# Kernel optimization log

Measured on AMD Instinct MI355X. Metric: run time of the kernel, lower is better.

The kernel has to match this reference:

```python
import jax, jax.numpy as jnp
import numpy as np

N = 50000
E = 1600000
F_IN = 4
F_OUT = 32
PERIODS = 12


def setup_inputs() -> dict:
    key = jax.random.key(0)
    ks = jax.random.split(key, 18)
    s_in = 1.0 / np.sqrt(F_IN)
    s_cat = 1.0 / np.sqrt(2 * F_OUT)
    s_out = 1.0 / np.sqrt(F_OUT)
    inp = {
        'x': jax.random.normal(ks[0], (N, F_IN, PERIODS), dtype=jnp.float32),
        'edge_index': jax.random.randint(ks[1], (2, E), 0, N, dtype=jnp.int32),
        'attention': jax.random.uniform(ks[2], (PERIODS,), dtype=jnp.float32),
        # GRU update gate z: GCNConv weight/bias + Linear(2*F_OUT -> F_OUT)
        'Wz': jax.random.normal(ks[3], (F_IN, F_OUT), jnp.float32) * s_in,
        'bz': jnp.zeros((F_OUT,), jnp.float32),
        'Lz': jax.random.normal(ks[4], (2 * F_OUT, F_OUT), jnp.float32) * s_cat,
        'lz': jnp.zeros((F_OUT,), jnp.float32),
        # reset gate r
        'Wr': jax.random.normal(ks[5], (F_IN, F_OUT), jnp.float32) * s_in,
        'br': jnp.zeros((F_OUT,), jnp.float32),
        'Lr': jax.random.normal(ks[6], (2 * F_OUT, F_OUT), jnp.float32) * s_cat,
        'lr': jnp.zeros((F_OUT,), jnp.float32),
        # candidate h
        'Wh': jax.random.normal(ks[7], (F_IN, F_OUT), jnp.float32) * s_in,
        'bh': jnp.zeros((F_OUT,), jnp.float32),
        'Lh': jax.random.normal(ks[8], (2 * F_OUT, F_OUT), jnp.float32) * s_cat,
        'lh': jnp.zeros((F_OUT,), jnp.float32),
        # outer Linear(32 -> periods)
        'Wo': jax.random.normal(ks[9], (F_OUT, PERIODS), jnp.float32) * s_out,
        'bo': jnp.zeros((PERIODS,), jnp.float32),
    }
    return inp


def reference(x, edge_index, attention, Wz, bz, Lz, lz, Wr, br, Lr, lr, Wh, bh, Lh, lh, Wo, bo):
    n = x.shape[0]
    # gcn_norm: add self loops, symmetric D^-1/2 (A+I) D^-1/2
    loop = jnp.arange(n, dtype=edge_index.dtype)
    row = jnp.concatenate([edge_index[0], loop])  # source
    col = jnp.concatenate([edge_index[1], loop])  # target
    w = jnp.ones(row.shape[0], dtype=x.dtype)
    deg = jax.ops.segment_sum(w, col, num_segments=n)
    dinv = jnp.where(deg > 0, jax.lax.rsqrt(deg), 0.0)
    norm = dinv[row] * dinv[col]  # [E+N]

    def conv(xt, W, b):
        h = xt @ W                                   # [N, F_OUT]
        msg = h[row] * norm[:, None]                 # gather + scale
        return jax.ops.segment_sum(msg, col, num_segments=n) + b

    H0 = jnp.zeros((n, F_OUT), dtype=x.dtype)  # A3TGCN passes H=None each period

    def tgcn(xt):
        Z = jax.nn.sigmoid(jnp.concatenate([conv(xt, Wz, bz), H0], axis=1) @ Lz + lz)
        R = jax.nn.sigmoid(jnp.concatenate([conv(xt, Wr, br), H0], axis=1) @ Lr + lr)
        Ht = jnp.tanh(jnp.concatenate([conv(xt, Wh, bh), H0 * R], axis=1) @ Lh + lh)
        return Z * H0 + (1.0 - Z) * Ht

    Hs = jax.vmap(tgcn)(jnp.moveaxis(x, 2, 0))       # [T, N, F_OUT]
    probs = jax.nn.softmax(attention)
    H = jnp.einsum('tnc,t->nc', Hs, probs)           # attention-weighted sum over periods
    return jax.nn.relu(H) @ Wo + bo                  # [N, PERIODS]
```

## Files before the change

### kernel.cpp

```cpp
#include <hip/hip_runtime.h>
#include <hip/hip_fp16.h>
#include <math.h>

#define CHUNK 6144
#define CAPG  10240
#define GNODES 21

union U2H { uint2 u; __half2 h[2]; };

__global__ void k_pre(const float* __restrict__ Wz, const float* __restrict__ Lz, const float* __restrict__ lz,
                      const float* __restrict__ Wh, const float* __restrict__ Lh, const float* __restrict__ lh,
                      const float* __restrict__ bz, const float* __restrict__ bh,
                      const float* __restrict__ att,
                      float* __restrict__ AzT, float* __restrict__ AhT,
                      float* __restrict__ bzp, float* __restrict__ bhp, float* __restrict__ probs,
                      int* __restrict__ gcur) {
  int t = threadIdx.x;
  gcur[t] = 0;
  if (t < 128) {
    int f = t >> 2, k = t & 3;
    float s = 0.f, s2 = 0.f;
    for (int j = 0; j < 32; ++j) {
      s  = fmaf(Wz[k * 32 + j], Lz[j * 32 + f], s);
      s2 = fmaf(Wh[k * 32 + j], Lh[j * 32 + f], s2);
    }
    AzT[t] = s; AhT[t] = s2;
  }
  if (t >= 128 && t < 160) {
    int f = t - 128;
    float s = lz[f], s2 = lh[f];
    for (int j = 0; j < 32; ++j) {
      s  = fmaf(bz[j], Lz[j * 32 + f], s);
      s2 = fmaf(bh[j], Lh[j * 32 + f], s2);
    }
    bzp[f] = s; bhp[f] = s2;
  }
  if (t == 160) {
    float m = att[0];
    for (int i = 1; i < 12; ++i) m = fmaxf(m, att[i]);
    float e[12]; float s = 0.f;
    for (int i = 0; i < 12; ++i) { e[i] = __expf(att[i] - m); s += e[i]; }
    for (int i = 0; i < 12; ++i) probs[i] = e[i] / s;
  }
}

__global__ __launch_bounds__(1024) void k_part(const int* __restrict__ row, const int* __restrict__ col,
                                               int E, int nbkt,
                                               int* __restrict__ gcur, unsigned* __restrict__ part) {
  __shared__ unsigned spak[CHUNK];
  __shared__ unsigned char sbkt[CHUNK];
  __shared__ unsigned char slc[CHUNK];
  __shared__ int hist[256], sscan[256], scur[256], gbase[256];
  int t = threadIdx.x;
  int base = blockIdx.x * CHUNK;
  int cnt = E - base; if (cnt > CHUNK) cnt = CHUNK;
  if (t < 256) hist[t] = 0;
  __syncthreads();
  for (int i = t; i < cnt; i += 1024) {
    int c = col[base + i];
    int b = c >> 8;
    sbkt[i] = (unsigned char)b;
    slc[i]  = (unsigned char)(c & 255);
    atomicAdd(&hist[b], 1);
  }
  __syncthreads();
  int v = 0;
  if (t < 256) { v = hist[t]; sscan[t] = v; }
  __syncthreads();
  for (int off = 1; off < 256; off <<= 1) {
    int a = 0;
    if (t < 256 && t >= off) a = sscan[t - off];
    __syncthreads();
    if (t < 256) sscan[t] += a;
    __syncthreads();
  }
  if (t < 256) {
    sscan[t] -= v;
    gbase[t] = (v > 0) ? atomicAdd(&gcur[t], v) : 0;
    scur[t] = 0;
  }
  __syncthreads();
  for (int i = t; i < cnt; i += 1024) {
    int r = row[base + i];
    int b = sbkt[i];
    int pos = atomicAdd(&scur[b], 1);
    spak[sscan[b] + pos] = ((unsigned)r << 8) | (unsigned)slc[i];
  }
  __syncthreads();
  int wave = t >> 6, lane = t & 63;
  for (int b = wave; b < nbkt; b += 16) {
    int len = hist[b], gb = gbase[b], src = sscan[b];
    int lim = CAPG - gb; if (lim > len) lim = len;
    unsigned* dst = part + (size_t)b * CAPG + gb;
    for (int j = lane; j < lim; j += 64) dst[j] = spak[src + j];
  }
}

__global__ __launch_bounds__(1024) void k_sort(const unsigned* __restrict__ part, const int* __restrict__ gcur,
                                               const float4* __restrict__ x4,
                                               int* __restrict__ csr, int2* __restrict__ rng,
                                               float* __restrict__ dinv, uint2* __restrict__ xh2, int n) {
  __shared__ unsigned sedge[CAPG];
  __shared__ int hist[256], soff[256], scur2[256];
  __shared__ float sdi[256];
  int b = blockIdx.x, t = threadIdx.x;
  int cnt = gcur[b]; if (cnt > CAPG) cnt = CAPG;
  const unsigned* src = part + (size_t)b * CAPG;
  if (t < 256) hist[t] = 0;
  __syncthreads();
  for (int i = t; i < cnt; i += 1024) {
    unsigned e = src[i];
    sedge[i] = e;
    atomicAdd(&hist[e & 255u], 1);
  }
  __syncthreads();
  int v = 0;
  if (t < 256) { v = hist[t]; soff[t] = v; }
  __syncthreads();
  for (int off = 1; off < 256; off <<= 1) {
    int a = 0;
    if (t < 256 && t >= off) a = soff[t - off];
    __syncthreads();
    if (t < 256) soff[t] += a;
    __syncthreads();
  }
  int base = b * CAPG;
  if (t < 256) {
    int excl = soff[t] - v;
    int node = b * 256 + t;
    float di = rsqrtf((float)(v + 1));
    sdi[t] = di;
    if (node < n) {
      rng[node] = make_int2(base + excl, base + excl + v);
      dinv[node] = di;
    }
    soff[t] = excl;
    scur2[t] = 0;
  }
  __syncthreads();
  for (int i = t; i < cnt; i += 1024) {
    unsigned e = sedge[i];
    int lc = (int)(e & 255u);
    int pos = atomicAdd(&scur2[lc], 1);
    csr[base + soff[lc] + pos] = (int)(e >> 8);
  }
  int gb = b * 3072;
  for (int j = t; j < 3072; j += 1024) {
    int gi = gb + j;
    if (gi < n * 12) {
      float4 f = x4[gi];
      float d = sdi[j / 12];
      __half2 h0 = __floats2half2_rn(d * f.x, d * f.y);
      __half2 h1 = __floats2half2_rn(d * f.z, d * f.w);
      uint2 u; u.x = *(unsigned*)&h0; u.y = *(unsigned*)&h1;
      xh2[gi] = u;
    }
  }
}

__global__ __launch_bounds__(256) void k_gather(const int* __restrict__ csr, const int2* __restrict__ rng,
                                                const float* __restrict__ dinv, const uint2* __restrict__ xh2,
                                                const float* __restrict__ AzT, const float* __restrict__ AhT,
                                                const float* __restrict__ bzp, const float* __restrict__ bhp,
                                                const float* __restrict__ probs,
                                                const float* __restrict__ Wo, const float* __restrict__ bo,
                                                float* __restrict__ out, int n) {
  __shared__ float sY[GNODES * 49];
  __shared__ float sH[GNODES * 33];
  __shared__ float4 sAz4[32], sAh4[32];
  __shared__ float sbzp[32], sbhp[32], sprobs[12], sbo[12], sWo[384];
  int t = threadIdx.x;
  int nb = blockIdx.x * GNODES;

  if (t < 32) {
    sAz4[t] = ((const float4*)AzT)[t];
    sAh4[t] = ((const float4*)AhT)[t];
    sbzp[t] = bzp[t]; sbhp[t] = bhp[t];
  }
  if (t >= 32 && t < 44) { sprobs[t - 32] = probs[t - 32]; sbo[t - 32] = bo[t - 32]; }
  for (int i = t; i < 384; i += 256) sWo[i] = Wo[i];

  int grp = t / 12, c = t - grp * 12;
  int node = nb + grp;
  if (grp < GNODES && node < n) {
    U2H s; s.u = xh2[(size_t)node * 12 + c];
    float2 f0 = __half22float2(s.h[0]), f1 = __half22float2(s.h[1]);
    float a0 = f0.x, a1 = f0.y, a2 = f1.x, a3 = f1.y;
    int2 r = rng[node];
    int e = r.x, end = r.y;
#define ACC4(V) { \
    float2 g0 = __half22float2(V.h[0]), g1 = __half22float2(V.h[1]); \
    a0 += g0.x; a1 += g0.y; a2 += g1.x; a3 += g1.y; }
    for (; e + 8 <= end; e += 8) {
      int r0 = csr[e],     r1 = csr[e + 1], r2 = csr[e + 2], r3 = csr[e + 3];
      int r4 = csr[e + 4], r5 = csr[e + 5], r6 = csr[e + 6], r7 = csr[e + 7];
      U2H v0, v1, v2, v3, v4, v5, v6, v7;
      v0.u = xh2[(size_t)r0 * 12 + c];
      v1.u = xh2[(size_t)r1 * 12 + c];
      v2.u = xh2[(size_t)r2 * 12 + c];
      v3.u = xh2[(size_t)r3 * 12 + c];
      v4.u = xh2[(size_t)r4 * 12 + c];
      v5.u = xh2[(size_t)r5 * 12 + c];
      v6.u = xh2[(size_t)r6 * 12 + c];
      v7.u = xh2[(size_t)r7 * 12 + c];
      ACC4(v0) ACC4(v1) ACC4(v2) ACC4(v3) ACC4(v4) ACC4(v5) ACC4(v6) ACC4(v7)
    }
    for (; e < end; ++e) {
      int r0 = csr[e];
      U2H v0; v0.u = xh2[(size_t)r0 * 12 + c];
      ACC4(v0)
    }
#undef ACC4
    float di = dinv[node];
    float* yb = sY + grp * 49 + c * 4;
    yb[0] = a0 * di; yb[1] = a1 * di; yb[2] = a2 * di; yb[3] = a3 * di;
  }
  __syncthreads();

  for (int u = t; u < GNODES * 32; u += 256) {
    int ln = u >> 5, f = u & 31;
    if (nb + ln >= n) continue;
    const float* y = sY + ln * 49;
    float4 az = sAz4[f], ah = sAh4[f];
    float bzf = sbzp[f], bhf = sbhp[f];
    float acc = 0.f;
#pragma unroll
    for (int tt = 0; tt < 12; ++tt) {
      float y0 = y[tt], y1 = y[12 + tt], y2 = y[24 + tt], y3 = y[36 + tt];
      float za = fmaf(az.x, y0, fmaf(az.y, y1, fmaf(az.z, y2, fmaf(az.w, y3, bzf))));
      float ha = fmaf(ah.x, y0, fmaf(ah.y, y1, fmaf(ah.z, y2, fmaf(ah.w, y3, bhf))));
      float ez = __expf(za);
      float ax = fabsf(ha);
      float e2 = __expf(-2.f * ax);
      float g = (1.f - e2) / ((1.f + ez) * (1.f + e2));
      acc = fmaf(sprobs[tt], copysignf(g, ha), acc);
    }
    sH[ln * 33 + f] = fmaxf(acc, 0.f);
  }
  __syncthreads();

  if (t < GNODES * 12) {
    int ln = t / 12, p = t - ln * 12;
    int node2 = nb + ln;
    if (node2 < n) {
      float acc = sbo[p];
      const float* h = sH + ln * 33;
      const float* wv = sWo + p;
#pragma unroll
      for (int f2 = 0; f2 < 32; ++f2) acc = fmaf(h[f2], wv[f2 * 12], acc);
      out[node2 * 12 + p] = acc;
    }
  }
}

extern "C" void kernel_launch(void* const* d_in, const int* in_sizes, int n_in,
                              void* d_out, int out_size, void* d_ws, size_t ws_size,
                              hipStream_t stream) {
  const float* x   = (const float*)d_in[0];
  const int*   ei  = (const int*)d_in[1];
  const float* att = (const float*)d_in[2];
  const float* Wz  = (const float*)d_in[3];
  const float* bz  = (const float*)d_in[4];
  const float* Lz  = (const float*)d_in[5];
  const float* lz  = (const float*)d_in[6];
  const float* Wh  = (const float*)d_in[11];
  const float* bh  = (const float*)d_in[12];
  const float* Lh  = (const float*)d_in[13];
  const float* lh  = (const float*)d_in[14];
  const float* Wo  = (const float*)d_in[15];
  const float* bo  = (const float*)d_in[16];
  float* out = (float*)d_out;

  const int N = in_sizes[0] / (4 * 12);
  const int E = in_sizes[1] / 2;
  const int NBKT = (N + 255) >> 8;
  const int* row = ei;
  const int* col = ei + E;

  char* w = (char*)d_ws;
  size_t o = 0;
  auto alloc = [&](size_t bytes) -> char* {
    o = (o + 255) & ~(size_t)255;
    char* p = w + o; o += bytes; return p;
  };
  float* pAzT   = (float*)alloc(128 * 4);
  float* pAhT   = (float*)alloc(128 * 4);
  float* pbzp   = (float*)alloc(32 * 4);
  float* pbhp   = (float*)alloc(32 * 4);
  float* pprobs = (float*)alloc(12 * 4);
  int*   pgcur  = (int*)alloc(256 * 4);
  float* pdinv  = (float*)alloc((size_t)NBKT * 256 * 4);
  int2*  prng   = (int2*)alloc((size_t)N * 8);
  unsigned* ppart = (unsigned*)alloc((size_t)256 * CAPG * 4);
  int*   pcsr   = (int*)alloc((size_t)256 * CAPG * 4);
  uint2* pxh    = (uint2*)alloc((size_t)NBKT * 256 * 12 * 8);
  (void)ws_size; (void)n_in; (void)out_size;

  k_pre<<<1, 256, 0, stream>>>(Wz, Lz, lz, Wh, Lh, lh, bz, bh, att,
                               pAzT, pAhT, pbzp, pbhp, pprobs, pgcur);
  k_part<<<(E + CHUNK - 1) / CHUNK, 1024, 0, stream>>>(row, col, E, NBKT, pgcur, ppart);
  k_sort<<<NBKT, 1024, 0, stream>>>(ppart, pgcur, (const float4*)x, pcsr, prng, pdinv, pxh, N);
  k_gather<<<(N + GNODES - 1) / GNODES, 256, 0, stream>>>(pcsr, prng, pdinv, pxh,
                                                          pAzT, pAhT, pbzp, pbhp, pprobs,
                                                          Wo, bo, out, N);
}
```

Measured before the change: 170.5 us.

## Replace CSR sort and gather with per-bucket shared-memory atomic accumulation

Drops the per-bucket counting sort that built a CSR array and per-node ranges. The first kernel now only counts degrees and builds the scaled half-precision features. The aggregation kernel splits each 256-node bucket across four blocks; each block scans the bucket's whole partitioned edge list, keeps only edges whose target falls in its 64-node slice, and adds 16-byte neighbour feature chunks into shared memory with atomics. This removes the sort pass and the CSR write and read. In exchange, each block reads its bucket's edge list redundantly, pays for shared-memory float atomics, and the grid becomes much smaller than the old gather launch.

```diff
diff --git a/kernel.cpp b/kernel.cpp
--- a/kernel.cpp
+++ b/kernel.cpp
@@ -4,9 +4,11 @@
 
 #define CHUNK 6144
 #define CAPG  10240
-#define GNODES 21
+#define SPLIT 4
+#define SUBN  64
 
 union U2H { uint2 u; __half2 h[2]; };
+union U4H { uint4 u; __half2 h[4]; };
 
 __global__ void k_pre(const float* __restrict__ Wz, const float* __restrict__ Lz, const float* __restrict__ lz,
                       const float* __restrict__ Wh, const float* __restrict__ Lh, const float* __restrict__ lh,
@@ -96,54 +98,25 @@
   }
 }
 
-__global__ __launch_bounds__(1024) void k_sort(const unsigned* __restrict__ part, const int* __restrict__ gcur,
-                                               const float4* __restrict__ x4,
-                                               int* __restrict__ csr, int2* __restrict__ rng,
-                                               float* __restrict__ dinv, uint2* __restrict__ xh2, int n) {
-  __shared__ unsigned sedge[CAPG];
-  __shared__ int hist[256], soff[256], scur2[256];
+__global__ __launch_bounds__(1024) void k_deg_xh(const unsigned* __restrict__ part, const int* __restrict__ gcur,
+                                                 const float4* __restrict__ x4,
+                                                 float* __restrict__ dinv, uint2* __restrict__ xh2, int n) {
+  __shared__ int hist[256];
   __shared__ float sdi[256];
   int b = blockIdx.x, t = threadIdx.x;
   int cnt = gcur[b]; if (cnt > CAPG) cnt = CAPG;
   const unsigned* src = part + (size_t)b * CAPG;
   if (t < 256) hist[t] = 0;
   __syncthreads();
-  for (int i = t; i < cnt; i += 1024) {
-    unsigned e = src[i];
-    sedge[i] = e;
-    atomicAdd(&hist[e & 255u], 1);
-  }
-  __syncthreads();
-  int v = 0;
-  if (t < 256) { v = hist[t]; soff[t] = v; }
-  __syncthreads();
-  for (int off = 1; off < 256; off <<= 1) {
-    int a = 0;
-    if (t < 256 && t >= off) a = soff[t - off];
-    __syncthreads();
-    if (t < 256) soff[t] += a;
-    __syncthreads();
-  }
-  int base = b * CAPG;
+  for (int i = t; i < cnt; i += 1024) atomicAdd(&hist[src[i] & 255u], 1);
+  __syncthreads();
   if (t < 256) {
-    int excl = soff[t] - v;
     int node = b * 256 + t;
-    float di = rsqrtf((float)(v + 1));
+    float di = rsqrtf((float)(hist[t] + 1));
     sdi[t] = di;
-    if (node < n) {
-      rng[node] = make_int2(base + excl, base + excl + v);
-      dinv[node] = di;
-    }
-    soff[t] = excl;
-    scur2[t] = 0;
-  }
-  __syncthreads();
-  for (int i = t; i < cnt; i += 1024) {
-    unsigned e = sedge[i];
-    int lc = (int)(e & 255u);
-    int pos = atomicAdd(&scur2[lc], 1);
-    csr[base + soff[lc] + pos] = (int)(e >> 8);
-  }
+    if (node < n) dinv[node] = di;
+  }
+  __syncthreads();
   int gb = b * 3072;
   for (int j = t; j < 3072; j += 1024) {
     int gi = gb + j;
@@ -158,19 +131,21 @@
   }
 }
 
-__global__ __launch_bounds__(256) void k_gather(const int* __restrict__ csr, const int2* __restrict__ rng,
-                                                const float* __restrict__ dinv, const uint2* __restrict__ xh2,
+__global__ __launch_bounds__(256, 6) void k_acc(const unsigned* __restrict__ part, const int* __restrict__ gcur,
+                                                const float* __restrict__ dinv, const uint4* __restrict__ xh4,
                                                 const float* __restrict__ AzT, const float* __restrict__ AhT,
                                                 const float* __restrict__ bzp, const float* __restrict__ bhp,
                                                 const float* __restrict__ probs,
                                                 const float* __restrict__ Wo, const float* __restrict__ bo,
                                                 float* __restrict__ out, int n) {
-  __shared__ float sY[GNODES * 49];
-  __shared__ float sH[GNODES * 33];
+  __shared__ float sAcc[SUBN * 49];
+  __shared__ float sdi[SUBN];
   __shared__ float4 sAz4[32], sAh4[32];
   __shared__ float sbzp[32], sbhp[32], sprobs[12], sbo[12], sWo[384];
   int t = threadIdx.x;
-  int nb = blockIdx.x * GNODES;
+  int b   = blockIdx.x >> 2;
+  int sub = blockIdx.x & 3;
+  int nb = b * 256 + sub * SUBN;
 
   if (t < 32) {
     sAz4[t] = ((const float4*)AzT)[t];
@@ -179,51 +154,68 @@
   }
   if (t >= 32 && t < 44) { sprobs[t - 32] = probs[t - 32]; sbo[t - 32] = bo[t - 32]; }
   for (int i = t; i < 384; i += 256) sWo[i] = Wo[i];
-
-  int grp = t / 12, c = t - grp * 12;
-  int node = nb + grp;
-  if (grp < GNODES && node < n) {
-    U2H s; s.u = xh2[(size_t)node * 12 + c];
-    float2 f0 = __half22float2(s.h[0]), f1 = __half22float2(s.h[1]);
-    float a0 = f0.x, a1 = f0.y, a2 = f1.x, a3 = f1.y;
-    int2 r = rng[node];
-    int e = r.x, end = r.y;
-#define ACC4(V) { \
-    float2 g0 = __half22float2(V.h[0]), g1 = __half22float2(V.h[1]); \
-    a0 += g0.x; a1 += g0.y; a2 += g1.x; a3 += g1.y; }
-    for (; e + 8 <= end; e += 8) {
-      int r0 = csr[e],     r1 = csr[e + 1], r2 = csr[e + 2], r3 = csr[e + 3];
-      int r4 = csr[e + 4], r5 = csr[e + 5], r6 = csr[e + 6], r7 = csr[e + 7];
-      U2H v0, v1, v2, v3, v4, v5, v6, v7;
-      v0.u = xh2[(size_t)r0 * 12 + c];
-      v1.u = xh2[(size_t)r1 * 12 + c];
-      v2.u = xh2[(size_t)r2 * 12 + c];
-      v3.u = xh2[(size_t)r3 * 12 + c];
-      v4.u = xh2[(size_t)r4 * 12 + c];
-      v5.u = xh2[(size_t)r5 * 12 + c];
-      v6.u = xh2[(size_t)r6 * 12 + c];
-      v7.u = xh2[(size_t)r7 * 12 + c];
-      ACC4(v0) ACC4(v1) ACC4(v2) ACC4(v3) ACC4(v4) ACC4(v5) ACC4(v6) ACC4(v7)
-    }
-    for (; e < end; ++e) {
-      int r0 = csr[e];
-      U2H v0; v0.u = xh2[(size_t)r0 * 12 + c];
-      ACC4(v0)
-    }
-#undef ACC4
-    float di = dinv[node];
-    float* yb = sY + grp * 49 + c * 4;
-    yb[0] = a0 * di; yb[1] = a1 * di; yb[2] = a2 * di; yb[3] = a3 * di;
-  }
-  __syncthreads();
-
-  for (int u = t; u < GNODES * 32; u += 256) {
+  if (t < SUBN) {
+    int node = nb + t;
+    sdi[t] = (node < n) ? dinv[node] : 0.f;
+  }
+  for (int k = t; k < SUBN * 6; k += 256) {
+    int ln = k / 6, cc = k % 6;
+    int node = nb + ln;
+    float* ap = sAcc + ln * 49 + cc * 8;
+    if (node < n) {
+      U4H v; v.u = xh4[(size_t)node * 6 + cc];
+      float2 f0 = __half22float2(v.h[0]), f1 = __half22float2(v.h[1]);
+      float2 f2 = __half22float2(v.h[2]), f3 = __half22float2(v.h[3]);
+      ap[0] = f0.x; ap[1] = f0.y; ap[2] = f1.x; ap[3] = f1.y;
+      ap[4] = f2.x; ap[5] = f2.y; ap[6] = f3.x; ap[7] = f3.y;
+    } else {
+      ap[0] = 0.f; ap[1] = 0.f; ap[2] = 0.f; ap[3] = 0.f;
+      ap[4] = 0.f; ap[5] = 0.f; ap[6] = 0.f; ap[7] = 0.f;
+    }
+  }
+  __syncthreads();
+
+  int cnt = gcur[b]; if (cnt > CAPG) cnt = CAPG;
+  const unsigned* src = part + (size_t)b * CAPG;
+  const int NG = 42;
+  int g = t / 6, c = t - g * 6;
+#define PROC(e) { \
+    int lc = (int)((e) & 255u); \
+    if ((lc >> 6) == sub) { \
+      U4H v; v.u = xh4[(size_t)((e) >> 8) * 6 + c]; \
+      float* ap = sAcc + (lc & 63) * 49 + c * 8; \
+      float2 f0 = __half22float2(v.h[0]), f1 = __half22float2(v.h[1]); \
+      float2 f2 = __half22float2(v.h[2]), f3 = __half22float2(v.h[3]); \
+      atomicAdd(ap + 0, f0.x); atomicAdd(ap + 1, f0.y); \
+      atomicAdd(ap + 2, f1.x); atomicAdd(ap + 3, f1.y); \
+      atomicAdd(ap + 4, f2.x); atomicAdd(ap + 5, f2.y); \
+      atomicAdd(ap + 6, f3.x); atomicAdd(ap + 7, f3.y); \
+    } }
+  if (g < NG) {
+    int i = g;
+    for (; i + 3 * NG < cnt; i += 4 * NG) {
+      unsigned e0 = src[i], e1 = src[i + NG], e2 = src[i + 2 * NG], e3 = src[i + 3 * NG];
+      PROC(e0) PROC(e1) PROC(e2) PROC(e3)
+    }
+    for (; i < cnt; i += NG) { unsigned e = src[i]; PROC(e) }
+  }
+#undef PROC
+  __syncthreads();
+
+  for (int k = t; k < SUBN * 48; k += 256) {
+    int ln = k / 48, m = k - ln * 48;
+    sAcc[ln * 49 + m] *= sdi[ln];
+  }
+  __syncthreads();
+
+  for (int k = 0; k < 8; ++k) {
+    int u = t + k * 256;
     int ln = u >> 5, f = u & 31;
-    if (nb + ln >= n) continue;
-    const float* y = sY + ln * 49;
+    bool valid = (nb + ln < n);
+    const float* y = sAcc + ln * 49;
     float4 az = sAz4[f], ah = sAh4[f];
     float bzf = sbzp[f], bhf = sbhp[f];
-    float acc = 0.f;
+    float acc2 = 0.f;
 #pragma unroll
     for (int tt = 0; tt < 12; ++tt) {
       float y0 = y[tt], y1 = y[12 + tt], y2 = y[24 + tt], y3 = y[36 + tt];
@@ -232,23 +224,25 @@
       float ez = __expf(za);
       float ax = fabsf(ha);
       float e2 = __expf(-2.f * ax);
-      float g = (1.f - e2) / ((1.f + ez) * (1.f + e2));
-      acc = fmaf(sprobs[tt], copysignf(g, ha), acc);
-    }
-    sH[ln * 33 + f] = fmaxf(acc, 0.f);
-  }
-  __syncthreads();
-
-  if (t < GNODES * 12) {
-    int ln = t / 12, p = t - ln * 12;
-    int node2 = nb + ln;
-    if (node2 < n) {
-      float acc = sbo[p];
-      const float* h = sH + ln * 33;
+      float gg = (1.f - e2) / ((1.f + ez) * (1.f + e2));
+      acc2 = fmaf(sprobs[tt], copysignf(gg, ha), acc2);
+    }
+    __syncthreads();
+    if (valid) sAcc[ln * 49 + f] = fmaxf(acc2, 0.f);
+  }
+  __syncthreads();
+
+  for (int k = 0; k < 3; ++k) {
+    int u = t + k * 256;
+    int ln = u / 12, p = u - ln * 12;
+    int node = nb + ln;
+    if (node < n) {
+      float s = sbo[p];
+      const float* h = sAcc + ln * 49;
       const float* wv = sWo + p;
 #pragma unroll
-      for (int f2 = 0; f2 < 32; ++f2) acc = fmaf(h[f2], wv[f2 * 12], acc);
-      out[node2 * 12 + p] = acc;
+      for (int f2 = 0; f2 < 32; ++f2) s = fmaf(h[f2], wv[f2 * 12], s);
+      out[node * 12 + p] = s;
     }
   }
 }
@@ -290,17 +284,15 @@
   float* pprobs = (float*)alloc(12 * 4);
   int*   pgcur  = (int*)alloc(256 * 4);
   float* pdinv  = (float*)alloc((size_t)NBKT * 256 * 4);
-  int2*  prng   = (int2*)alloc((size_t)N * 8);
   unsigned* ppart = (unsigned*)alloc((size_t)256 * CAPG * 4);
-  int*   pcsr   = (int*)alloc((size_t)256 * CAPG * 4);
   uint2* pxh    = (uint2*)alloc((size_t)NBKT * 256 * 12 * 8);
   (void)ws_size; (void)n_in; (void)out_size;
 
   k_pre<<<1, 256, 0, stream>>>(Wz, Lz, lz, Wh, Lh, lh, bz, bh, att,
                                pAzT, pAhT, pbzp, pbhp, pprobs, pgcur);
   k_part<<<(E + CHUNK - 1) / CHUNK, 1024, 0, stream>>>(row, col, E, NBKT, pgcur, ppart);
-  k_sort<<<NBKT, 1024, 0, stream>>>(ppart, pgcur, (const float4*)x, pcsr, prng, pdinv, pxh, N);
-  k_gather<<<(N + GNODES - 1) / GNODES, 256, 0, stream>>>(pcsr, prng, pdinv, pxh,
-                                                          pAzT, pAhT, pbzp, pbhp, pprobs,
-                                                          Wo, bo, out, N);
-}
+  k_deg_xh<<<NBKT, 1024, 0, stream>>>(ppart, pgcur, (const float4*)x, pdinv, pxh, N);
+  k_acc<<<NBKT * SPLIT, 256, 0, stream>>>(ppart, pgcur, pdinv, (const uint4*)pxh,
+                                          pAzT, pAhT, pbzp, pbhp, pprobs,
+                                          Wo, bo, out, N);
+}
```

After: 652.3 us. 3.83x slower.

## Replace two-pass bucket sort CSR build with padded per-node atomic scatter

Applied to the files above, without the earlier changes.

Drops the partition and sort kernels and builds a fixed-width adjacency table (128 slots per node) with one global atomicAdd per edge, which also yields each node's degree. The scaled half-precision features move to a separate elementwise kernel, and the gather reads neighbour indices with int4 loads and computes the degree normaliser inline. This removes the shared-memory histograms, scans and sync-heavy sorting in exchange for contention on global atomics, scattered writes, and a larger padded table. Any node with more than 128 in-edges is silently truncated, and neighbour order becomes nondeterministic.

```diff
diff --git a/kernel.cpp b/kernel.cpp
--- a/kernel.cpp
+++ b/kernel.cpp
@@ -2,21 +2,22 @@
 #include <hip/hip_fp16.h>
 #include <math.h>
 
-#define CHUNK 6144
-#define CAPG  10240
+#define PADN   128
 #define GNODES 21
 
 union U2H { uint2 u; __half2 h[2]; };
 
-__global__ void k_pre(const float* __restrict__ Wz, const float* __restrict__ Lz, const float* __restrict__ lz,
+__global__ __launch_bounds__(1024) void k_pre(const float* __restrict__ Wz, const float* __restrict__ Lz, const float* __restrict__ lz,
                       const float* __restrict__ Wh, const float* __restrict__ Lh, const float* __restrict__ lh,
                       const float* __restrict__ bz, const float* __restrict__ bh,
                       const float* __restrict__ att,
                       float* __restrict__ AzT, float* __restrict__ AhT,
                       float* __restrict__ bzp, float* __restrict__ bhp, float* __restrict__ probs,
-                      int* __restrict__ gcur) {
+                      int* __restrict__ cnt, int n) {
+  int gid = blockIdx.x * 1024 + threadIdx.x;
+  if (gid < n) cnt[gid] = 0;
+  if (blockIdx.x != 0) return;
   int t = threadIdx.x;
-  gcur[t] = 0;
   if (t < 128) {
     int f = t >> 2, k = t & 3;
     float s = 0.f, s2 = 0.f;
@@ -25,8 +26,7 @@
       s2 = fmaf(Wh[k * 32 + j], Lh[j * 32 + f], s2);
     }
     AzT[t] = s; AhT[t] = s2;
-  }
-  if (t >= 128 && t < 160) {
+  } else if (t < 160) {
     int f = t - 128;
     float s = lz[f], s2 = lh[f];
     for (int j = 0; j < 32; ++j) {
@@ -34,8 +34,7 @@
       s2 = fmaf(bh[j], Lh[j * 32 + f], s2);
     }
     bzp[f] = s; bhp[f] = s2;
-  }
-  if (t == 160) {
+  } else if (t == 160) {
     float m = att[0];
     for (int i = 1; i < 12; ++i) m = fmaxf(m, att[i]);
     float e[12]; float s = 0.f;
@@ -44,122 +43,45 @@
   }
 }
 
-__global__ __launch_bounds__(1024) void k_part(const int* __restrict__ row, const int* __restrict__ col,
-                                               int E, int nbkt,
-                                               int* __restrict__ gcur, unsigned* __restrict__ part) {
-  __shared__ unsigned spak[CHUNK];
-  __shared__ unsigned char sbkt[CHUNK];
-  __shared__ unsigned char slc[CHUNK];
-  __shared__ int hist[256], sscan[256], scur[256], gbase[256];
-  int t = threadIdx.x;
-  int base = blockIdx.x * CHUNK;
-  int cnt = E - base; if (cnt > CHUNK) cnt = CHUNK;
-  if (t < 256) hist[t] = 0;
-  __syncthreads();
-  for (int i = t; i < cnt; i += 1024) {
-    int c = col[base + i];
-    int b = c >> 8;
-    sbkt[i] = (unsigned char)b;
-    slc[i]  = (unsigned char)(c & 255);
-    atomicAdd(&hist[b], 1);
-  }
-  __syncthreads();
-  int v = 0;
-  if (t < 256) { v = hist[t]; sscan[t] = v; }
-  __syncthreads();
-  for (int off = 1; off < 256; off <<= 1) {
-    int a = 0;
-    if (t < 256 && t >= off) a = sscan[t - off];
-    __syncthreads();
-    if (t < 256) sscan[t] += a;
-    __syncthreads();
-  }
-  if (t < 256) {
-    sscan[t] -= v;
-    gbase[t] = (v > 0) ? atomicAdd(&gcur[t], v) : 0;
-    scur[t] = 0;
-  }
-  __syncthreads();
-  for (int i = t; i < cnt; i += 1024) {
-    int r = row[base + i];
-    int b = sbkt[i];
-    int pos = atomicAdd(&scur[b], 1);
-    spak[sscan[b] + pos] = ((unsigned)r << 8) | (unsigned)slc[i];
-  }
-  __syncthreads();
-  int wave = t >> 6, lane = t & 63;
-  for (int b = wave; b < nbkt; b += 16) {
-    int len = hist[b], gb = gbase[b], src = sscan[b];
-    int lim = CAPG - gb; if (lim > len) lim = len;
-    unsigned* dst = part + (size_t)b * CAPG + gb;
-    for (int j = lane; j < lim; j += 64) dst[j] = spak[src + j];
-  }
-}
-
-__global__ __launch_bounds__(1024) void k_sort(const unsigned* __restrict__ part, const int* __restrict__ gcur,
-                                               const float4* __restrict__ x4,
-                                               int* __restrict__ csr, int2* __restrict__ rng,
-                                               float* __restrict__ dinv, uint2* __restrict__ xh2, int n) {
-  __shared__ unsigned sedge[CAPG];
-  __shared__ int hist[256], soff[256], scur2[256];
-  __shared__ float sdi[256];
-  int b = blockIdx.x, t = threadIdx.x;
-  int cnt = gcur[b]; if (cnt > CAPG) cnt = CAPG;
-  const unsigned* src = part + (size_t)b * CAPG;
-  if (t < 256) hist[t] = 0;
-  __syncthreads();
-  for (int i = t; i < cnt; i += 1024) {
-    unsigned e = src[i];
-    sedge[i] = e;
-    atomicAdd(&hist[e & 255u], 1);
-  }
-  __syncthreads();
-  int v = 0;
-  if (t < 256) { v = hist[t]; soff[t] = v; }
-  __syncthreads();
-  for (int off = 1; off < 256; off <<= 1) {
-    int a = 0;
-    if (t < 256 && t >= off) a = soff[t - off];
-    __syncthreads();
-    if (t < 256) soff[t] += a;
-    __syncthreads();
-  }
-  int base = b * CAPG;
-  if (t < 256) {
-    int excl = soff[t] - v;
-    int node = b * 256 + t;
-    float di = rsqrtf((float)(v + 1));
-    sdi[t] = di;
-    if (node < n) {
-      rng[node] = make_int2(base + excl, base + excl + v);
-      dinv[node] = di;
-    }
-    soff[t] = excl;
-    scur2[t] = 0;
-  }
-  __syncthreads();
-  for (int i = t; i < cnt; i += 1024) {
-    unsigned e = sedge[i];
-    int lc = (int)(e & 255u);
-    int pos = atomicAdd(&scur2[lc], 1);
-    csr[base + soff[lc] + pos] = (int)(e >> 8);
-  }
-  int gb = b * 3072;
-  for (int j = t; j < 3072; j += 1024) {
-    int gi = gb + j;
-    if (gi < n * 12) {
-      float4 f = x4[gi];
-      float d = sdi[j / 12];
-      __half2 h0 = __floats2half2_rn(d * f.x, d * f.y);
-      __half2 h1 = __floats2half2_rn(d * f.z, d * f.w);
-      uint2 u; u.x = *(unsigned*)&h0; u.y = *(unsigned*)&h1;
-      xh2[gi] = u;
-    }
-  }
-}
-
-__global__ __launch_bounds__(256) void k_gather(const int* __restrict__ csr, const int2* __restrict__ rng,
-                                                const float* __restrict__ dinv, const uint2* __restrict__ xh2,
+__global__ __launch_bounds__(256) void k_scatter(const int* __restrict__ row, const int* __restrict__ col,
+                                                 int E, int* __restrict__ cnt, int* __restrict__ csr) {
+  int i = (blockIdx.x * 256 + threadIdx.x) * 4;
+  if (i + 3 < E) {
+    int4 c4 = *(const int4*)(col + i);
+    int4 r4 = *(const int4*)(row + i);
+    int p0 = atomicAdd(&cnt[c4.x], 1);
+    int p1 = atomicAdd(&cnt[c4.y], 1);
+    int p2 = atomicAdd(&cnt[c4.z], 1);
+    int p3 = atomicAdd(&cnt[c4.w], 1);
+    if (p0 < PADN) csr[c4.x * PADN + p0] = r4.x;
+    if (p1 < PADN) csr[c4.y * PADN + p1] = r4.y;
+    if (p2 < PADN) csr[c4.z * PADN + p2] = r4.z;
+    if (p3 < PADN) csr[c4.w * PADN + p3] = r4.w;
+  } else {
+    for (; i < E; ++i) {
+      int c = col[i], r = row[i];
+      int p = atomicAdd(&cnt[c], 1);
+      if (p < PADN) csr[c * PADN + p] = r;
+    }
+  }
+}
+
+__global__ __launch_bounds__(1024) void k_dx(const float4* __restrict__ x4, const int* __restrict__ cnt,
+                                             uint2* __restrict__ xh2, int n12) {
+  int gid = blockIdx.x * 1024 + threadIdx.x;
+  if (gid < n12) {
+    int node = gid / 12;
+    float d = rsqrtf((float)(cnt[node] + 1));
+    float4 f = x4[gid];
+    __half2 h0 = __floats2half2_rn(d * f.x, d * f.y);
+    __half2 h1 = __floats2half2_rn(d * f.z, d * f.w);
+    uint2 u; u.x = *(unsigned*)&h0; u.y = *(unsigned*)&h1;
+    xh2[gid] = u;
+  }
+}
+
+__global__ __launch_bounds__(256) void k_gather(const int* __restrict__ csr, const int* __restrict__ cnt,
+                                                const uint2* __restrict__ xh2,
                                                 const float* __restrict__ AzT, const float* __restrict__ AhT,
                                                 const float* __restrict__ bzp, const float* __restrict__ bhp,
                                                 const float* __restrict__ probs,
@@ -186,23 +108,24 @@
     U2H s; s.u = xh2[(size_t)node * 12 + c];
     float2 f0 = __half22float2(s.h[0]), f1 = __half22float2(s.h[1]);
     float a0 = f0.x, a1 = f0.y, a2 = f1.x, a3 = f1.y;
-    int2 r = rng[node];
-    int e = r.x, end = r.y;
+    int dg = cnt[node];
+    int e = node * PADN;
+    int end = e + (dg < PADN ? dg : PADN);
 #define ACC4(V) { \
     float2 g0 = __half22float2(V.h[0]), g1 = __half22float2(V.h[1]); \
     a0 += g0.x; a1 += g0.y; a2 += g1.x; a3 += g1.y; }
     for (; e + 8 <= end; e += 8) {
-      int r0 = csr[e],     r1 = csr[e + 1], r2 = csr[e + 2], r3 = csr[e + 3];
-      int r4 = csr[e + 4], r5 = csr[e + 5], r6 = csr[e + 6], r7 = csr[e + 7];
+      int4 ca = *(const int4*)(csr + e);
+      int4 cb = *(const int4*)(csr + e + 4);
       U2H v0, v1, v2, v3, v4, v5, v6, v7;
-      v0.u = xh2[(size_t)r0 * 12 + c];
-      v1.u = xh2[(size_t)r1 * 12 + c];
-      v2.u = xh2[(size_t)r2 * 12 + c];
-      v3.u = xh2[(size_t)r3 * 12 + c];
-      v4.u = xh2[(size_t)r4 * 12 + c];
-      v5.u = xh2[(size_t)r5 * 12 + c];
-      v6.u = xh2[(size_t)r6 * 12 + c];
-      v7.u = xh2[(size_t)r7 * 12 + c];
+      v0.u = xh2[(size_t)ca.x * 12 + c];
+      v1.u = xh2[(size_t)ca.y * 12 + c];
+      v2.u = xh2[(size_t)ca.z * 12 + c];
+      v3.u = xh2[(size_t)ca.w * 12 + c];
+      v4.u = xh2[(size_t)cb.x * 12 + c];
+      v5.u = xh2[(size_t)cb.y * 12 + c];
+      v6.u = xh2[(size_t)cb.z * 12 + c];
+      v7.u = xh2[(size_t)cb.w * 12 + c];
       ACC4(v0) ACC4(v1) ACC4(v2) ACC4(v3) ACC4(v4) ACC4(v5) ACC4(v6) ACC4(v7)
     }
     for (; e < end; ++e) {
@@ -211,7 +134,7 @@
       ACC4(v0)
     }
 #undef ACC4
-    float di = dinv[node];
+    float di = rsqrtf((float)(dg + 1));
     float* yb = sY + grp * 49 + c * 4;
     yb[0] = a0 * di; yb[1] = a1 * di; yb[2] = a2 * di; yb[3] = a3 * di;
   }
@@ -273,7 +196,6 @@
 
   const int N = in_sizes[0] / (4 * 12);
   const int E = in_sizes[1] / 2;
-  const int NBKT = (N + 255) >> 8;
   const int* row = ei;
   const int* col = ei + E;
 
@@ -288,19 +210,16 @@
   float* pbzp   = (float*)alloc(32 * 4);
   float* pbhp   = (float*)alloc(32 * 4);
   float* pprobs = (float*)alloc(12 * 4);
-  int*   pgcur  = (int*)alloc(256 * 4);
-  float* pdinv  = (float*)alloc((size_t)NBKT * 256 * 4);
-  int2*  prng   = (int2*)alloc((size_t)N * 8);
-  unsigned* ppart = (unsigned*)alloc((size_t)256 * CAPG * 4);
-  int*   pcsr   = (int*)alloc((size_t)256 * CAPG * 4);
-  uint2* pxh    = (uint2*)alloc((size_t)NBKT * 256 * 12 * 8);
+  int*   pcnt   = (int*)alloc((size_t)N * 4);
+  int*   pcsr   = (int*)alloc((size_t)N * PADN * 4);
+  uint2* pxh    = (uint2*)alloc((size_t)N * 12 * 8);
   (void)ws_size; (void)n_in; (void)out_size;
 
-  k_pre<<<1, 256, 0, stream>>>(Wz, Lz, lz, Wh, Lh, lh, bz, bh, att,
-                               pAzT, pAhT, pbzp, pbhp, pprobs, pgcur);
-  k_part<<<(E + CHUNK - 1) / CHUNK, 1024, 0, stream>>>(row, col, E, NBKT, pgcur, ppart);
-  k_sort<<<NBKT, 1024, 0, stream>>>(ppart, pgcur, (const float4*)x, pcsr, prng, pdinv, pxh, N);
-  k_gather<<<(N + GNODES - 1) / GNODES, 256, 0, stream>>>(pcsr, prng, pdinv, pxh,
+  k_pre<<<(N + 1023) / 1024, 1024, 0, stream>>>(Wz, Lz, lz, Wh, Lh, lh, bz, bh, att,
+                                                pAzT, pAhT, pbzp, pbhp, pprobs, pcnt, N);
+  k_scatter<<<(E / 4 + 255) / 256, 256, 0, stream>>>(row, col, E, pcnt, pcsr);
+  k_dx<<<(N * 12 + 1023) / 1024, 1024, 0, stream>>>((const float4*)x, pcnt, pxh, N * 12);
+  k_gather<<<(N + GNODES - 1) / GNODES, 256, 0, stream>>>(pcsr, pcnt, pxh,
                                                           pAzT, pAhT, pbzp, pbhp, pprobs,
                                                           Wo, bo, out, N);
 }
```

New measurement: 277.7 us. 62.9% more time.
